# Kernel tuning notes

Measured on AMD Instinct MI355X. Metric: run time of the kernel, lower is better.

Reference implementation:

```python
import jax, jax.numpy as jnp
import numpy as np
from jax import lax

# Constants matching PostProcess(conf_thres=0.4, iou_thres=0.5, merge=False, agnostic=False)
CONF_THRES = 0.4
IOU_THRES = 0.5
MAX_WH = 4096.0   # per-class box offset (agnostic=False)
MAX_DET = 300     # hardcoded in module
MAX_NMS = 30000   # cap on NMS candidates (yolov5 convention); JAX needs static shapes
B, N, NC = 16, 25200, 80


def setup_inputs() -> dict:
    key = jax.random.key(0)
    u = jax.random.uniform(key, (B, N, 5 + NC), dtype=jnp.float32)
    # cx,cy in [0,640); w,h in [2,102); obj and class scores in [0,1)
    scale = jnp.concatenate([jnp.array([640.0, 640.0, 100.0, 100.0], jnp.float32),
                             jnp.ones((1 + NC,), jnp.float32)])
    shift = jnp.concatenate([jnp.array([0.0, 0.0, 2.0, 2.0], jnp.float32),
                             jnp.zeros((1 + NC,), jnp.float32)])
    prediction = u * scale + shift
    return {"prediction": prediction}


def _cxcywh_to_xyxy(x):
    cx, cy, w, h = x[..., 0], x[..., 1], x[..., 2], x[..., 3]
    return jnp.stack([cx - 0.5 * w, cy - 0.5 * h, cx + 0.5 * w, cy + 0.5 * h], axis=-1)


def _process_one(x):  # x: [N, 5+NC]
    obj = x[:, 4]
    cls_conf = x[:, 5:] * obj[:, None]          # x[:,5:] *= x[:,4:5]
    box = _cxcywh_to_xyxy(x[:, :4])             # [N, 4]
    # multi-label candidate mask: obj > conf AND class conf > conf (x[xc] then x[:,5:] > conf)
    cand = (obj[:, None] > CONF_THRES) & (cls_conf > CONF_THRES)   # [N, NC]
    flat = jnp.where(cand, cls_conf, 0.0).reshape(-1)              # [N*NC]
    top_scores, top_idx = lax.top_k(flat, MAX_NMS)                 # static-size candidate set
    bi = top_idx // NC                                             # box index i
    cj = (top_idx % NC).astype(jnp.float32)                        # class index j
    cand_boxes = box[bi]                                           # [M, 4]
    scores0 = jnp.where(top_scores > CONF_THRES, top_scores, 0.0)  # 0 marks invalid/suppressed
    off_boxes = cand_boxes + cj[:, None] * MAX_WH                  # per-class offset for NMS
    areas = (off_boxes[:, 2] - off_boxes[:, 0]) * (off_boxes[:, 3] - off_boxes[:, 1])
    idx_range = jnp.arange(MAX_NMS)

    def step(scores, _):
        # greedy NMS: pick best remaining, suppress IoU > thresh (torchvision semantics)
        idx = jnp.argmax(scores)
        s = scores[idx]
        keep = s > 0.0
        b = off_boxes[idx]
        lt = jnp.maximum(b[:2], off_boxes[:, :2])
        rb = jnp.minimum(b[2:], off_boxes[:, 2:])
        wh = jnp.clip(rb - lt, 0.0)
        inter = wh[:, 0] * wh[:, 1]
        iou = inter / (areas[idx] + areas - inter + 1e-9)
        suppress = (iou > IOU_THRES) | (idx_range == idx)
        return jnp.where(suppress, 0.0, scores), (idx, keep)

    _, (keep_idx, keep_flag) = lax.scan(step, scores0, None, length=MAX_DET)
    rows = jnp.concatenate([cand_boxes[keep_idx],
                            top_scores[keep_idx][:, None],
                            cj[keep_idx][:, None]], axis=1)        # [MAX_DET, 6] = xyxy, conf, cls
    return jnp.where(keep_flag[:, None], rows, 0.0)


def reference(prediction):
    # Padded fixed-shape analogue of torch.stack(output): [B, MAX_DET, 6], zero rows = no detection
    return jax.vmap(_process_one)(prediction)
```

## Files before the change

### kernel.cpp

```cpp
#include <hip/hip_runtime.h>
#include <stdint.h>

#define BATCH 16
#define NROW 25200
#define NCLS 80
#define ROWF 85
#define MAXDET 300
#define MAXNMS 30000u
#define NBIN 3072
#define BASEBITS 0x3EC00000u
#define CAP 32768u
#define BATCH_FLOATS 2142000

#define PREBIN 2048
#define NBUCK 1024
#define BUCKCAP 256

#define GATHER_MIN 512u
#define SORTCAP 1024
#define CH_SZ 128

#define TILE_ROWS 80
#define TILE_FLOATS 6800
#define RPB 400
#define SUBT 5
#define SBLK 63

#define ROWS_PER_BLK 256
#define SBLK2 99

__device__ __forceinline__ bool iou_gt_half(float ax1, float ay1, float ax2, float ay2, float aa,
                                            float bx1, float by1, float bx2, float by2, float ba) {
    float ltx = fmaxf(ax1, bx1), lty = fmaxf(ay1, by1);
    float rbx = fminf(ax2, bx2), rby = fminf(ay2, by2);
    float wx = fmaxf(__fsub_rn(rbx, ltx), 0.0f);
    float wy = fmaxf(__fsub_rn(rby, lty), 0.0f);
    float inter = __fmul_rn(wx, wy);
    float den = __fadd_rn(__fsub_rn(__fadd_rn(aa, ba), inter), 1e-9f);
    float t = __fmul_rn(0.5f, den);
    if (!(inter > t)) return false;
    float tg = __fmul_rn(0.50000012f, den);
    if (inter >= tg) return true;
    return __fdiv_rn(inter, den) > 0.5f;
}

__global__ __launch_bounds__(256) void k_stage(const float* __restrict__ pred,
                                               unsigned* __restrict__ bcnt,
                                               unsigned long long* __restrict__ bucket,
                                               unsigned* __restrict__ oflow,
                                               int staged) {
    if (!staged) return;
    int bx = blockIdx.x;
    int b = bx / SBLK2, blk = bx - b * SBLK2;
    int t = threadIdx.x, lane = t & 63, wv = t >> 6;
    const float* pb = pred + (size_t)b * BATCH_FLOATS;
    unsigned* bc = bcnt + (size_t)b * NBUCK;
    unsigned long long* bk = bucket + (size_t)b * NBUCK * BUCKCAP;
    int r0 = blk * ROWS_PER_BLK + wv * 64;
    int rown = NROW - r0;
    if (rown <= 0) return;
    if (rown > 64) rown = 64;
    float obj = 0.0f;
    if (lane < rown) obj = pb[(size_t)(r0 + lane) * ROWF + 4];
    unsigned long long live = __ballot(obj > 0.4f);
    while (live) {
        int j = (int)__builtin_ctzll(live);
        live &= live - 1ULL;
        float o = __shfl(obj, j);
        const float* rp = pb + (size_t)(r0 + j) * ROWF;
        unsigned grow = (unsigned)(r0 + j);
        {
            float cv = rp[5 + lane];
            float s = __fmul_rn(cv, o);
            if (s >= 0.75f) {
                unsigned bits = __float_as_uint(s);
                unsigned bin = (bits - BASEBITS) >> 12;
                if (bin > (unsigned)(NBIN - 1)) bin = NBIN - 1;
                unsigned bb = bin - PREBIN;
                unsigned pos = atomicAdd(&bc[bb], 1u);
                if (pos < (unsigned)BUCKCAP) {
                    unsigned flat = grow * (unsigned)NCLS + (unsigned)lane;
                    bk[(size_t)bb * BUCKCAP + pos] =
                        ((unsigned long long)bits << 32) |
                        (unsigned long long)(0xFFFFFFFFu - flat);
                } else oflow[b] = 1u;
            }
        }
        if (lane < 16) {
            int c = 64 + lane;
            float cv = rp[5 + c];
            float s = __fmul_rn(cv, o);
            if (s >= 0.75f) {
                unsigned bits = __float_as_uint(s);
                unsigned bin = (bits - BASEBITS) >> 12;
                if (bin > (unsigned)(NBIN - 1)) bin = NBIN - 1;
                unsigned bb = bin - PREBIN;
                unsigned pos = atomicAdd(&bc[bb], 1u);
                if (pos < (unsigned)BUCKCAP) {
                    unsigned flat = grow * (unsigned)NCLS + (unsigned)c;
                    bk[(size_t)bb * BUCKCAP + pos] =
                        ((unsigned long long)bits << 32) |
                        (unsigned long long)(0xFFFFFFFFu - flat);
                } else oflow[b] = 1u;
            }
        }
    }
}

__global__ __launch_bounds__(256) void k_prep(const unsigned* __restrict__ bcnt,
                                              const unsigned* __restrict__ oflow,
                                              unsigned* __restrict__ suf2,
                                              int* __restrict__ meta,
                                              int staged) {
    __shared__ unsigned sh[NBUCK];
    __shared__ unsigned sS[NBUCK];
    __shared__ unsigned cs[256];
    __shared__ int s_cut, s_need, s_tot;
    int b = blockIdx.x, t = threadIdx.x;
    const unsigned* bc = bcnt + (size_t)b * NBUCK;
    for (int i = t; i < NBUCK; i += 256) sh[i] = bc[i];
    if (t == 0) { s_cut = -1; s_need = 0; s_tot = 0; }
    __syncthreads();
    const int CHUNK = NBUCK / 256;
    int base = t * CHUNK;
    unsigned tot = 0;
    for (int i = 0; i < CHUNK; ++i) tot += sh[base + i];
    cs[t] = tot;
    __syncthreads();
    for (int off = 1; off < 256; off <<= 1) {
        unsigned v = (t + off < 256) ? cs[t + off] : 0u;
        __syncthreads();
        cs[t] += v;
        __syncthreads();
    }
    unsigned after = (t + 1 < 256) ? cs[t + 1] : 0u;
    for (int i = CHUNK - 1; i >= 0; --i) {
        after += sh[base + i];
        sS[base + i] = after;
    }
    __syncthreads();
    unsigned* g2 = suf2 + (size_t)b * (NBUCK + 1);
    for (int i = t; i < NBUCK; i += 256) g2[i] = sS[i];
    if (t == 0) g2[NBUCK] = 0u;
    for (int i = 0; i < CHUNK; ++i) {
        int v = base + i;
        unsigned Sv = sS[v];
        unsigned Sn = (v + 1 < NBUCK) ? sS[v + 1] : 0u;
        if (Sv >= MAXNMS && Sn < MAXNMS) {
            s_cut = PREBIN + v;
            s_need = (int)(MAXNMS - Sn);
            s_tot = (int)Sv;
        }
    }
    __syncthreads();
    if (t == 0) {
        int valid = (staged && s_cut >= 0 && sS[0] >= MAXNMS && oflow[b] == 0u) ? 1 : 0;
        meta[b * 4 + 0] = valid ? s_cut : 0;
        meta[b * 4 + 1] = valid ? s_need : 0;
        meta[b * 4 + 2] = valid ? s_tot : 0;
        meta[b * 4 + 3] = valid;
    }
}

__global__ __launch_bounds__(256) void k_hist_fb(const float* __restrict__ pred,
                                                 unsigned* __restrict__ hist,
                                                 const int* __restrict__ meta) {
    int bx = blockIdx.x;
    int b = bx / SBLK, blk = bx - b * SBLK;
    if (meta[b * 4 + 3]) return;
    __shared__ __align__(16) float rows[TILE_FLOATS];
    __shared__ unsigned shist[NBIN];
    int t = threadIdx.x, lane = t & 63, wv = t >> 6;
    for (int i = t; i < NBIN; i += 256) shist[i] = 0u;
    const float* pbase = pred + (size_t)b * BATCH_FLOATS + (size_t)blk * RPB * ROWF;
    for (int st = 0; st < SUBT; ++st) {
        __syncthreads();
        const float4* src = (const float4*)(pbase + (size_t)st * TILE_ROWS * ROWF);
        float4* dst = (float4*)rows;
        for (int i = t; i < TILE_FLOATS / 4; i += 256) dst[i] = src[i];
        __syncthreads();
        for (int r = wv; r < TILE_ROWS; r += 4) {
            float obj = rows[r * ROWF + 4];
            if (!(obj > 0.4f)) continue;
            for (int half = 0; half < 2; ++half) {
                int c = lane + (half << 6);
                if (c < NCLS) {
                    float cv = rows[r * ROWF + 5 + c];
                    float s = __fmul_rn(cv, obj);
                    if (s > 0.4f) {
                        unsigned bits = __float_as_uint(s);
                        unsigned bin = (bits - BASEBITS) >> 12;
                        if (bin > (unsigned)(NBIN - 1)) bin = NBIN - 1;
                        atomicAdd(&shist[bin], 1u);
                    }
                }
            }
        }
    }
    __syncthreads();
    unsigned* gh = hist + (size_t)b * NBIN;
    for (int i = t; i < NBIN; i += 256) {
        unsigned v = shist[i];
        if (v) atomicAdd(&gh[i], v);
    }
}

__global__ __launch_bounds__(256) void k_scan_fb(const unsigned* __restrict__ hist,
                                                 unsigned* __restrict__ suf,
                                                 int* __restrict__ meta) {
    int b = blockIdx.x, t = threadIdx.x;
    if (meta[b * 4 + 3]) return;
    __shared__ unsigned sh[NBIN];
    __shared__ unsigned sS[NBIN];
    __shared__ unsigned cs[256];
    __shared__ int s_cut, s_need, s_tot;
    const unsigned* gh = hist + (size_t)b * NBIN;
    for (int i = t; i < NBIN; i += 256) sh[i] = gh[i];
    if (t == 0) { s_cut = 0; s_need = 0x7FFFFFFF; s_tot = 0; }
    __syncthreads();
    const int CHUNK = NBIN / 256;
    int base = t * CHUNK;
    unsigned tot = 0;
    for (int i = 0; i < CHUNK; ++i) tot += sh[base + i];
    cs[t] = tot;
    __syncthreads();
    for (int off = 1; off < 256; off <<= 1) {
        unsigned v = (t + off < 256) ? cs[t + off] : 0u;
        __syncthreads();
        cs[t] += v;
        __syncthreads();
    }
    unsigned after = (t + 1 < 256) ? cs[t + 1] : 0u;
    for (int i = CHUNK - 1; i >= 0; --i) {
        after += sh[base + i];
        sS[base + i] = after;
    }
    __syncthreads();
    unsigned* gs = suf + (size_t)b * (NBIN + 1);
    for (int i = t; i < NBIN; i += 256) gs[i] = sS[i];
    if (t == 0) gs[NBIN] = 0u;
    for (int i = 0; i < CHUNK; ++i) {
        int v = base + i;
        unsigned Sv = sS[v];
        unsigned Sn = (v + 1 < NBIN) ? sS[v + 1] : 0u;
        if (Sv >= MAXNMS && Sn < MAXNMS) {
            s_cut = v;
            s_need = (int)(MAXNMS - Sn);
            s_tot = (int)Sv;
        }
    }
    __syncthreads();
    if (t == 0) {
        int cut = s_cut, needv = s_need, totv = s_tot;
        if (sS[0] < MAXNMS) { cut = 0; needv = 0x7FFFFFFF; totv = (int)sS[0]; }
        meta[b * 4 + 0] = cut;
        meta[b * 4 + 1] = needv;
        meta[b * 4 + 2] = totv;
    }
}

__global__ __launch_bounds__(256) void k_scatter_fb(const float* __restrict__ pred,
                                                    const unsigned* __restrict__ suf,
                                                    const int* __restrict__ meta,
                                                    unsigned* __restrict__ cursor,
                                                    unsigned long long* __restrict__ keys) {
    int bx = blockIdx.x;
    int b = bx / SBLK, blk = bx - b * SBLK;
    if (meta[b * 4 + 3]) return;
    __shared__ __align__(16) float rows[TILE_FLOATS];
    int t = threadIdx.x, lane = t & 63, wv = t >> 6;
    int cutbin = meta[b * 4 + 0];
    const float* pbase = pred + (size_t)b * BATCH_FLOATS + (size_t)blk * RPB * ROWF;
    unsigned rowbase0 = (unsigned)(blk * RPB);
    const unsigned* gs = suf + (size_t)b * (NBIN + 1);
    unsigned* cur = cursor + (size_t)b * NBIN;
    unsigned long long* kb = keys + (size_t)b * CAP;
    for (int st = 0; st < SUBT; ++st) {
        __syncthreads();
        const float4* src = (const float4*)(pbase + (size_t)st * TILE_ROWS * ROWF);
        float4* dst = (float4*)rows;
        for (int i = t; i < TILE_FLOATS / 4; i += 256) dst[i] = src[i];
        __syncthreads();
        for (int r = wv; r < TILE_ROWS; r += 4) {
            float obj = rows[r * ROWF + 4];
            if (!(obj > 0.4f)) continue;
            unsigned grow = rowbase0 + (unsigned)(st * TILE_ROWS + r);
            for (int half = 0; half < 2; ++half) {
                int c = lane + (half << 6);
                if (c < NCLS) {
                    float cv = rows[r * ROWF + 5 + c];
                    float s = __fmul_rn(cv, obj);
                    if (s > 0.4f) {
                        unsigned bits = __float_as_uint(s);
                        unsigned bin = (bits - BASEBITS) >> 12;
                        if (bin > (unsigned)(NBIN - 1)) bin = NBIN - 1;
                        if ((int)bin >= cutbin) {
                            unsigned pos = gs[bin + 1] + atomicAdd(&cur[bin], 1u);
                            if (pos < CAP) {
                                unsigned flat = grow * (unsigned)NCLS + (unsigned)c;
                                kb[pos] = ((unsigned long long)bits << 32) |
                                          (unsigned long long)(0xFFFFFFFFu - flat);
                            }
                        }
                    }
                }
            }
        }
    }
}

__global__ __launch_bounds__(1024) void k_nms(const float* __restrict__ pred,
                                              const unsigned* __restrict__ suf,
                                              const unsigned* __restrict__ suf2,
                                              const int* __restrict__ meta,
                                              const unsigned long long* __restrict__ keys,
                                              const unsigned long long* __restrict__ bucket,
                                              float* __restrict__ out) {
    __shared__ unsigned sgsL[NBUCK + 1];
    __shared__ unsigned long long ktmp[SORTCAP];
    __shared__ unsigned long long skeys[SORTCAP];
    __shared__ unsigned maskW[CH_SZ][5];
    __shared__ unsigned sup0w[4];
    __shared__ float cbox[CH_SZ][9];
    __shared__ float kept[MAXDET][5];
    __shared__ int klist[MAXDET];
    __shared__ int s_nk, s_localk;

    int b = blockIdx.x;
    int tid = threadIdx.x;
    int lane = tid & 63, wv = tid >> 6;

    int cutbin = meta[b * 4 + 0];
    int needv  = meta[b * 4 + 1];
    unsigned total = (unsigned)meta[b * 4 + 2];
    int valid  = meta[b * 4 + 3];
    if (total > CAP) total = CAP;
    const unsigned* gs = suf + (size_t)b * (NBIN + 1);
    const unsigned* g2 = suf2 + (size_t)b * (NBUCK + 1);
    const unsigned long long* kb = keys + (size_t)b * CAP;
    const unsigned long long* bk = bucket + (size_t)b * NBUCK * BUCKCAP;
    const float* pb = pred + (size_t)b * BATCH_FLOATS;
    float* ob = out + (size_t)b * MAXDET * 6;

    if (valid) for (int i = tid; i < NBUCK + 1; i += 1024) sgsL[i] = g2[i];
    if (tid == 0) s_nk = 0;
    __syncthreads();

    unsigned limit;
    if (needv == 0x7FFFFFFF) limit = total;
    else limit = (valid ? sgsL[cutbin + 1 - PREBIN] : gs[cutbin + 1]) + (unsigned)needv;
    if (limit > total) limit = total;

#define GSV(v) (valid ? sgsL[(v) - PREBIN] : gs[(v)])

    unsigned p = 0;
    while (p < limit) {
        if (s_nk >= MAXDET) break;

        int lo = cutbin, hi = NBIN - 1, w1 = cutbin;
        while (lo <= hi) { int mid = (lo + hi) >> 1;
            if (GSV(mid) > p) { w1 = mid; lo = mid + 1; } else hi = mid - 1; }
        lo = cutbin; hi = NBIN - 1; int w2 = cutbin;
        while (lo <= hi) { int mid = (lo + hi) >> 1;
            if (GSV(mid) >= p + GATHER_MIN) { w2 = mid; lo = mid + 1; } else hi = mid - 1; }
        unsigned gEnd = GSV(w2);
        if (gEnd <= p) gEnd = GSV(cutbin);
        if (gEnd - p > (unsigned)SORTCAP) {
            if (w2 < w1) gEnd = GSV(w2 + 1);
            if (gEnd - p > (unsigned)SORTCAP) gEnd = p + SORTCAP;
        }
        unsigned G = gEnd - p;

        unsigned myLo = 0, myHi = 0;
        unsigned long long raw = 0ULL;
        if (tid < (int)G) {
            unsigned idx = p + (unsigned)tid;
            int l2 = cutbin, h2 = NBIN - 1, v = cutbin;
            while (l2 <= h2) { int mid = (l2 + h2) >> 1;
                if (GSV(mid) > idx) { v = mid; l2 = mid + 1; } else h2 = mid - 1; }
            unsigned bstart = GSV(v + 1);
            unsigned bend = GSV(v);
            unsigned e = idx - bstart;
            raw = valid ? bk[(size_t)(v - PREBIN) * BUCKCAP + e] : kb[idx];
            myLo = bstart - p;
            myHi = bend - p; if (myHi > G) myHi = G;
            ktmp[tid] = raw;
        }
        __syncthreads();
        if (tid < (int)G) {
            unsigned rank = 0;
            for (unsigned u = myLo; u < myHi; ++u) rank += (ktmp[u] > raw) ? 1u : 0u;
            skeys[myLo + rank] = raw;
        }
        __syncthreads();

        unsigned consumable = limit - p; if (consumable > G) consumable = G;

        for (unsigned c0 = 0; c0 < consumable; c0 += CH_SZ) {
            int nk0 = s_nk;
            if (nk0 >= MAXDET) break;
            int CH = (int)((consumable - c0 < (unsigned)CH_SZ) ? (consumable - c0) : (unsigned)CH_SZ);

            if (tid < CH_SZ * 5) maskW[tid / 5][tid % 5] = 0u;
            if (tid >= CH_SZ * 5 && tid < CH_SZ * 5 + 4) sup0w[tid - CH_SZ * 5] = 0u;
            if (tid < CH) {
                unsigned long long kk = skeys[c0 + tid];
                unsigned flat = 0xFFFFFFFFu - (unsigned)kk;
                unsigned bi = flat / (unsigned)NCLS;
                unsigned cc = flat - bi * (unsigned)NCLS;
                const float* rp = pb + (size_t)bi * ROWF;
                float cx = rp[0], cy = rp[1], wd = rp[2], ht = rp[3];
                float hw = __fmul_rn(0.5f, wd), hh = __fmul_rn(0.5f, ht);
                float off = __fmul_rn((float)cc, 4096.0f);
                float x1 = __fsub_rn(cx, hw), y1 = __fsub_rn(cy, hh);
                float x2 = __fadd_rn(cx, hw), y2 = __fadd_rn(cy, hh);
                float ox1 = __fadd_rn(x1, off), oy1 = __fadd_rn(y1, off);
                float ox2 = __fadd_rn(x2, off), oy2 = __fadd_rn(y2, off);
                cbox[tid][0] = ox1; cbox[tid][1] = oy1;
                cbox[tid][2] = ox2; cbox[tid][3] = oy2;
                cbox[tid][4] = __fmul_rn(__fsub_rn(ox2, ox1), __fsub_rn(oy2, oy1));
            }
            __syncthreads();

            {
                int col = tid & (CH_SZ - 1);
                int part = tid >> 7;
                if (col < CH) {
                    float bx1 = cbox[col][0], by1 = cbox[col][1];
                    float bx2 = cbox[col][2], by2 = cbox[col][3], ba = cbox[col][4];
                    unsigned part16 = 0u;
                    int rbase = part << 4;
                    for (int k = 0; k < 16; ++k) {
                        int i2 = rbase + k;
                        if (i2 >= col || i2 >= CH) break;
                        if (iou_gt_half(cbox[i2][0], cbox[i2][1], cbox[i2][2], cbox[i2][3],
                                        cbox[i2][4], bx1, by1, bx2, by2, ba))
                            part16 |= (1u << k);
                    }
                    if (part16)
                        atomicOr(&maskW[col][part >> 1], part16 << ((part & 1) << 4));
                    bool f = false;
                    for (int k2 = part; k2 < nk0; k2 += 8) {
                        if (iou_gt_half(kept[k2][0], kept[k2][1], kept[k2][2], kept[k2][3],
                                        kept[k2][4], bx1, by1, bx2, by2, ba)) f = true;
                    }
                    if (f) atomicOr(&sup0w[col >> 5], 1u << (col & 31));
                }
            }
            __syncthreads();

            if (wv == 0) {
                unsigned keptw = 0u;
                int nkv = nk0, lk = 0;
                unsigned pre0 = (lane < 4 && CH > 0) ? maskW[0][lane] : 0u;
                unsigned pre1 = (lane < 4 && CH > 1) ? maskW[1][lane] : 0u;
                for (int j = 0; j < CH && nkv < MAXDET; ++j) {
                    unsigned colw = pre0;
                    pre0 = pre1;
                    pre1 = (lane < 4 && (j + 2) < CH) ? maskW[j + 2][lane] : 0u;
                    bool hit = (keptw & colw) != 0u;
                    bool sup = __any(hit);
                    if ((sup0w[j >> 5] >> (j & 31)) & 1u) sup = true;
                    if (!sup) {
                        if (lane == (j >> 5)) keptw |= 1u << (j & 31);
                        if (lane == 0) klist[lk] = j;
                        lk++; nkv++;
                    }
                }
                if (lane == 0) { s_localk = lk; s_nk = nkv; }
            }
            __syncthreads();

            int lk = s_localk;
            for (int t2 = tid; t2 < lk; t2 += 1024) {
                int i = klist[t2];
                int oidx = nk0 + t2;
                kept[oidx][0] = cbox[i][0]; kept[oidx][1] = cbox[i][1];
                kept[oidx][2] = cbox[i][2]; kept[oidx][3] = cbox[i][3];
                kept[oidx][4] = cbox[i][4];
                unsigned long long kk = skeys[c0 + i];
                unsigned bits = (unsigned)(kk >> 32);
                unsigned flat = 0xFFFFFFFFu - (unsigned)kk;
                unsigned bi = flat / (unsigned)NCLS;
                unsigned cc = flat - bi * (unsigned)NCLS;
                const float* rp = pb + (size_t)bi * ROWF;
                float cx = rp[0], cy = rp[1], wd = rp[2], ht = rp[3];
                float hw = __fmul_rn(0.5f, wd), hh = __fmul_rn(0.5f, ht);
                float* orow = ob + (size_t)oidx * 6;
                orow[0] = __fsub_rn(cx, hw);
                orow[1] = __fsub_rn(cy, hh);
                orow[2] = __fadd_rn(cx, hw);
                orow[3] = __fadd_rn(cy, hh);
                orow[4] = __uint_as_float(bits);
                orow[5] = (float)cc;
            }
            __syncthreads();
        }
        p = gEnd;
    }
#undef GSV
}

extern "C" void kernel_launch(void* const* d_in, const int* in_sizes, int n_in,
                              void* d_out, int out_size, void* d_ws, size_t ws_size,
                              hipStream_t stream) {
    const float* pred = (const float*)d_in[0];
    float* outp = (float*)d_out;
    char* ws = (char*)d_ws;

    const size_t OFF_KEYS = 0;
    const size_t SZ_KEYS  = (size_t)BATCH * CAP * 8;
    const size_t OFF_HIST = OFF_KEYS + SZ_KEYS;
    const size_t SZ_HIST  = (size_t)BATCH * NBIN * 4;
    const size_t OFF_CUR  = OFF_HIST + SZ_HIST;
    const size_t SZ_CUR   = (size_t)BATCH * NBIN * 4;
    const size_t OFF_BCNT = OFF_CUR + SZ_CUR;
    const size_t SZ_BCNT  = (size_t)BATCH * NBUCK * 4;
    const size_t OFF_OFLW = OFF_BCNT + SZ_BCNT;
    const size_t SZ_OFLW  = (size_t)BATCH * 4;
    const size_t OFF_META = OFF_OFLW + SZ_OFLW;
    const size_t SZ_META  = (size_t)BATCH * 4 * 4;
    const size_t OFF_SUF  = OFF_META + SZ_META;
    const size_t SZ_SUF   = (size_t)BATCH * (NBIN + 1) * 4;
    const size_t OFF_SUF2 = OFF_SUF + SZ_SUF;
    const size_t SZ_SUF2  = (size_t)BATCH * (NBUCK + 1) * 4;
    const size_t OFF_BUCK = OFF_SUF2 + SZ_SUF2;
    const size_t SZ_BUCK  = (size_t)BATCH * NBUCK * BUCKCAP * 8;
    const size_t WS_NEEDED = OFF_BUCK + SZ_BUCK;

    int staged = (ws_size >= WS_NEEDED) ? 1 : 0;

    unsigned long long* keys   = (unsigned long long*)(ws + OFF_KEYS);
    unsigned* hist             = (unsigned*)(ws + OFF_HIST);
    unsigned* cursor           = (unsigned*)(ws + OFF_CUR);
    unsigned* bcnt             = (unsigned*)(ws + OFF_BCNT);
    unsigned* oflow            = (unsigned*)(ws + OFF_OFLW);
    int* meta                  = (int*)(ws + OFF_META);
    unsigned* suf              = (unsigned*)(ws + OFF_SUF);
    unsigned* suf2             = (unsigned*)(ws + OFF_SUF2);
    unsigned long long* bucket = (unsigned long long*)(ws + OFF_BUCK);

    hipMemsetAsync(ws + OFF_HIST, 0, SZ_HIST + SZ_CUR + SZ_BCNT + SZ_OFLW + SZ_META, stream);
    hipMemsetAsync(d_out, 0, (size_t)out_size * sizeof(float), stream);

    k_stage<<<dim3(BATCH * SBLK2), dim3(256), 0, stream>>>(pred, bcnt, bucket, oflow, staged);
    k_prep<<<dim3(BATCH), dim3(256), 0, stream>>>(bcnt, oflow, suf2, meta, staged);
    k_hist_fb<<<dim3(BATCH * SBLK), dim3(256), 0, stream>>>(pred, hist, meta);
    k_scan_fb<<<dim3(BATCH), dim3(256), 0, stream>>>(hist, suf, meta);
    k_scatter_fb<<<dim3(BATCH * SBLK), dim3(256), 0, stream>>>(pred, suf, meta, cursor, keys);
    k_nms<<<dim3(BATCH), dim3(1024), 0, stream>>>(pred, suf, suf2, meta, keys, bucket, outp);
}
```

Measured before the change: 360.4 us.

## Replace global bucket atomics with per-block shared histograms and compact candidate list

The staging kernel now builds a per-block shared-memory histogram and a local key buffer, then writes per-block histograms and appends its keys to one compact per-batch candidate array with a single global atomic. k_prep sums the per-block histograms and checks that no bucket exceeds the sort capacity. In the staged path, the NMS kernel rescans the whole candidate list for each window, filters keys by bin range, and ranks them within their bin. This removes heavy global atomic contention and the large sparse bucket array. The cost is a full candidate scan per window inside the single-block-per-batch NMS kernel, plus extra histogram traffic.

```diff
diff --git a/kernel.cpp b/kernel.cpp
--- a/kernel.cpp
+++ b/kernel.cpp
@@ -14,7 +14,8 @@
 
 #define PREBIN 2048
 #define NBUCK 1024
-#define BUCKCAP 256
+#define CANDCAP 131072u
+#define KMAX 2048u
 
 #define GATHER_MIN 512u
 #define SORTCAP 1024
@@ -44,70 +45,93 @@
     return __fdiv_rn(inter, den) > 0.5f;
 }
 
+__device__ __forceinline__ unsigned bin_of_bits(unsigned bits) {
+    unsigned v = (bits - BASEBITS) >> 12;
+    if (v > (unsigned)(NBIN - 1)) v = NBIN - 1;
+    return v;
+}
+
 __global__ __launch_bounds__(256) void k_stage(const float* __restrict__ pred,
-                                               unsigned* __restrict__ bcnt,
-                                               unsigned long long* __restrict__ bucket,
+                                               unsigned* __restrict__ ghist,
+                                               unsigned* __restrict__ ccnt,
+                                               unsigned long long* __restrict__ cand,
                                                unsigned* __restrict__ oflow,
                                                int staged) {
     if (!staged) return;
+    __shared__ unsigned shist[NBUCK];
+    __shared__ unsigned long long skey[KMAX];
+    __shared__ unsigned s_cnt, s_n, s_base;
     int bx = blockIdx.x;
     int b = bx / SBLK2, blk = bx - b * SBLK2;
     int t = threadIdx.x, lane = t & 63, wv = t >> 6;
+    for (int i = t; i < NBUCK; i += 256) shist[i] = 0u;
+    if (t == 0) s_cnt = 0u;
+    __syncthreads();
     const float* pb = pred + (size_t)b * BATCH_FLOATS;
-    unsigned* bc = bcnt + (size_t)b * NBUCK;
-    unsigned long long* bk = bucket + (size_t)b * NBUCK * BUCKCAP;
     int r0 = blk * ROWS_PER_BLK + wv * 64;
     int rown = NROW - r0;
-    if (rown <= 0) return;
-    if (rown > 64) rown = 64;
-    float obj = 0.0f;
-    if (lane < rown) obj = pb[(size_t)(r0 + lane) * ROWF + 4];
-    unsigned long long live = __ballot(obj > 0.4f);
-    while (live) {
-        int j = (int)__builtin_ctzll(live);
-        live &= live - 1ULL;
-        float o = __shfl(obj, j);
-        const float* rp = pb + (size_t)(r0 + j) * ROWF;
-        unsigned grow = (unsigned)(r0 + j);
-        {
-            float cv = rp[5 + lane];
-            float s = __fmul_rn(cv, o);
-            if (s >= 0.75f) {
-                unsigned bits = __float_as_uint(s);
-                unsigned bin = (bits - BASEBITS) >> 12;
-                if (bin > (unsigned)(NBIN - 1)) bin = NBIN - 1;
-                unsigned bb = bin - PREBIN;
-                unsigned pos = atomicAdd(&bc[bb], 1u);
-                if (pos < (unsigned)BUCKCAP) {
+    if (rown > 0) {
+        if (rown > 64) rown = 64;
+        float obj = 0.0f;
+        if (lane < rown) obj = pb[(size_t)(r0 + lane) * ROWF + 4];
+        unsigned long long live = __ballot(obj > 0.4f);
+        while (live) {
+            int j = (int)__builtin_ctzll(live);
+            live &= live - 1ULL;
+            float o = __shfl(obj, j);
+            const float* rp = pb + (size_t)(r0 + j) * ROWF;
+            unsigned grow = (unsigned)(r0 + j);
+            {
+                float s = __fmul_rn(rp[5 + lane], o);
+                if (s >= 0.75f) {
+                    unsigned bits = __float_as_uint(s);
+                    unsigned bin = bin_of_bits(bits);
+                    atomicAdd(&shist[bin - PREBIN], 1u);
+                    unsigned u = atomicAdd(&s_cnt, 1u);
                     unsigned flat = grow * (unsigned)NCLS + (unsigned)lane;
-                    bk[(size_t)bb * BUCKCAP + pos] =
-                        ((unsigned long long)bits << 32) |
-                        (unsigned long long)(0xFFFFFFFFu - flat);
-                } else oflow[b] = 1u;
-            }
-        }
-        if (lane < 16) {
-            int c = 64 + lane;
-            float cv = rp[5 + c];
-            float s = __fmul_rn(cv, o);
-            if (s >= 0.75f) {
-                unsigned bits = __float_as_uint(s);
-                unsigned bin = (bits - BASEBITS) >> 12;
-                if (bin > (unsigned)(NBIN - 1)) bin = NBIN - 1;
-                unsigned bb = bin - PREBIN;
-                unsigned pos = atomicAdd(&bc[bb], 1u);
-                if (pos < (unsigned)BUCKCAP) {
+                    if (u < KMAX)
+                        skey[u] = ((unsigned long long)bits << 32) |
+                                  (unsigned long long)(0xFFFFFFFFu - flat);
+                    else oflow[b] = 1u;
+                }
+            }
+            if (lane < 16) {
+                int c = 64 + lane;
+                float s = __fmul_rn(rp[5 + c], o);
+                if (s >= 0.75f) {
+                    unsigned bits = __float_as_uint(s);
+                    unsigned bin = bin_of_bits(bits);
+                    atomicAdd(&shist[bin - PREBIN], 1u);
+                    unsigned u = atomicAdd(&s_cnt, 1u);
                     unsigned flat = grow * (unsigned)NCLS + (unsigned)c;
-                    bk[(size_t)bb * BUCKCAP + pos] =
-                        ((unsigned long long)bits << 32) |
-                        (unsigned long long)(0xFFFFFFFFu - flat);
-                } else oflow[b] = 1u;
-            }
-        }
-    }
-}
-
-__global__ __launch_bounds__(256) void k_prep(const unsigned* __restrict__ bcnt,
+                    if (u < KMAX)
+                        skey[u] = ((unsigned long long)bits << 32) |
+                                  (unsigned long long)(0xFFFFFFFFu - flat);
+                    else oflow[b] = 1u;
+                }
+            }
+        }
+    }
+    __syncthreads();
+    unsigned* gh = ghist + (size_t)(b * SBLK2 + blk) * NBUCK;
+    for (int i = t; i < NBUCK; i += 256) gh[i] = shist[i];
+    if (t == 0) {
+        unsigned n = s_cnt;
+        if (n > KMAX) n = KMAX;
+        unsigned base = atomicAdd(&ccnt[b], n);
+        if (base + n > CANDCAP) oflow[b] = 1u;
+        s_n = n; s_base = base;
+    }
+    __syncthreads();
+    unsigned n = s_n, base = s_base;
+    if (base + n <= CANDCAP) {
+        unsigned long long* cd = cand + (size_t)b * CANDCAP + base;
+        for (unsigned k = t; k < n; k += 256) cd[k] = skey[k];
+    }
+}
+
+__global__ __launch_bounds__(256) void k_prep(const unsigned* __restrict__ ghist,
+                                              const unsigned* __restrict__ ccnt,
                                               const unsigned* __restrict__ oflow,
                                               unsigned* __restrict__ suf2,
                                               int* __restrict__ meta,
@@ -116,11 +140,18 @@
     __shared__ unsigned sS[NBUCK];
     __shared__ unsigned cs[256];
     __shared__ int s_cut, s_need, s_tot;
+    __shared__ unsigned s_bad;
     int b = blockIdx.x, t = threadIdx.x;
-    const unsigned* bc = bcnt + (size_t)b * NBUCK;
-    for (int i = t; i < NBUCK; i += 256) sh[i] = bc[i];
-    if (t == 0) { s_cut = -1; s_need = 0; s_tot = 0; }
-    __syncthreads();
+    for (int i = t; i < NBUCK; i += 256) {
+        unsigned s = 0;
+        const unsigned* g = ghist + (size_t)b * SBLK2 * NBUCK + i;
+        for (int k = 0; k < SBLK2; ++k) s += g[(size_t)k * NBUCK];
+        sh[i] = s;
+    }
+    if (t == 0) { s_cut = -1; s_need = 0; s_tot = 0; s_bad = 0u; }
+    __syncthreads();
+    for (int i = t; i < NBUCK; i += 256)
+        if (sh[i] > (unsigned)SORTCAP) atomicOr(&s_bad, 1u);
     const int CHUNK = NBUCK / 256;
     int base = t * CHUNK;
     unsigned tot = 0;
@@ -154,7 +185,8 @@
     }
     __syncthreads();
     if (t == 0) {
-        int valid = (staged && s_cut >= 0 && sS[0] >= MAXNMS && oflow[b] == 0u) ? 1 : 0;
+        int valid = (staged && s_cut >= 0 && s_bad == 0u &&
+                     oflow[b] == 0u && ccnt[b] <= CANDCAP) ? 1 : 0;
         meta[b * 4 + 0] = valid ? s_cut : 0;
         meta[b * 4 + 1] = valid ? s_need : 0;
         meta[b * 4 + 2] = valid ? s_tot : 0;
@@ -187,12 +219,7 @@
                 if (c < NCLS) {
                     float cv = rows[r * ROWF + 5 + c];
                     float s = __fmul_rn(cv, obj);
-                    if (s > 0.4f) {
-                        unsigned bits = __float_as_uint(s);
-                        unsigned bin = (bits - BASEBITS) >> 12;
-                        if (bin > (unsigned)(NBIN - 1)) bin = NBIN - 1;
-                        atomicAdd(&shist[bin], 1u);
-                    }
+                    if (s > 0.4f) atomicAdd(&shist[bin_of_bits(__float_as_uint(s))], 1u);
                 }
             }
         }
@@ -292,8 +319,7 @@
                     float s = __fmul_rn(cv, obj);
                     if (s > 0.4f) {
                         unsigned bits = __float_as_uint(s);
-                        unsigned bin = (bits - BASEBITS) >> 12;
-                        if (bin > (unsigned)(NBIN - 1)) bin = NBIN - 1;
+                        unsigned bin = bin_of_bits(bits);
                         if ((int)bin >= cutbin) {
                             unsigned pos = gs[bin + 1] + atomicAdd(&cur[bin], 1u);
                             if (pos < CAP) {
@@ -313,8 +339,9 @@
                                               const unsigned* __restrict__ suf,
                                               const unsigned* __restrict__ suf2,
                                               const int* __restrict__ meta,
+                                              const unsigned* __restrict__ ccnt,
                                               const unsigned long long* __restrict__ keys,
-                                              const unsigned long long* __restrict__ bucket,
+                                              const unsigned long long* __restrict__ cand,
                                               float* __restrict__ out) {
     __shared__ unsigned sgsL[NBUCK + 1];
     __shared__ unsigned long long ktmp[SORTCAP];
@@ -325,6 +352,7 @@
     __shared__ float kept[MAXDET][5];
     __shared__ int klist[MAXDET];
     __shared__ int s_nk, s_localk;
+    __shared__ unsigned s_gc;
 
     int b = blockIdx.x;
     int tid = threadIdx.x;
@@ -334,11 +362,13 @@
     int needv  = meta[b * 4 + 1];
     unsigned total = (unsigned)meta[b * 4 + 2];
     int valid  = meta[b * 4 + 3];
-    if (total > CAP) total = CAP;
+    if (!valid && total > CAP) total = CAP;
     const unsigned* gs = suf + (size_t)b * (NBIN + 1);
     const unsigned* g2 = suf2 + (size_t)b * (NBUCK + 1);
     const unsigned long long* kb = keys + (size_t)b * CAP;
-    const unsigned long long* bk = bucket + (size_t)b * NBUCK * BUCKCAP;
+    const unsigned long long* cd = cand + (size_t)b * CANDCAP;
+    unsigned ccb = valid ? ccnt[b] : 0u;
+    if (ccb > CANDCAP) ccb = CANDCAP;
     const float* pb = pred + (size_t)b * BATCH_FLOATS;
     float* ob = out + (size_t)b * MAXDET * 6;
 
@@ -346,12 +376,12 @@
     if (tid == 0) s_nk = 0;
     __syncthreads();
 
+#define GSV(v) (valid ? sgsL[(v) - PREBIN] : gs[(v)])
+
     unsigned limit;
     if (needv == 0x7FFFFFFF) limit = total;
-    else limit = (valid ? sgsL[cutbin + 1 - PREBIN] : gs[cutbin + 1]) + (unsigned)needv;
+    else limit = GSV(cutbin + 1) + (unsigned)needv;
     if (limit > total) limit = total;
-
-#define GSV(v) (valid ? sgsL[(v) - PREBIN] : gs[(v)])
 
     unsigned p = 0;
     while (p < limit) {
@@ -371,28 +401,55 @@
         }
         unsigned G = gEnd - p;
 
-        unsigned myLo = 0, myHi = 0;
-        unsigned long long raw = 0ULL;
-        if (tid < (int)G) {
-            unsigned idx = p + (unsigned)tid;
-            int l2 = cutbin, h2 = NBIN - 1, v = cutbin;
-            while (l2 <= h2) { int mid = (l2 + h2) >> 1;
-                if (GSV(mid) > idx) { v = mid; l2 = mid + 1; } else h2 = mid - 1; }
-            unsigned bstart = GSV(v + 1);
-            unsigned bend = GSV(v);
-            unsigned e = idx - bstart;
-            raw = valid ? bk[(size_t)(v - PREBIN) * BUCKCAP + e] : kb[idx];
-            myLo = bstart - p;
-            myHi = bend - p; if (myHi > G) myHi = G;
-            ktmp[tid] = raw;
-        }
-        __syncthreads();
-        if (tid < (int)G) {
-            unsigned rank = 0;
-            for (unsigned u = myLo; u < myHi; ++u) rank += (ktmp[u] > raw) ? 1u : 0u;
-            skeys[myLo + rank] = raw;
-        }
-        __syncthreads();
+        if (valid) {
+            if (tid == 0) s_gc = 0u;
+            __syncthreads();
+            for (unsigned k = tid; k < ccb; k += 1024) {
+                unsigned long long key = cd[k];
+                unsigned v = bin_of_bits((unsigned)(key >> 32));
+                if ((int)v >= w2 && (int)v <= w1) {
+                    unsigned u = atomicAdd(&s_gc, 1u);
+                    if (u < (unsigned)SORTCAP) ktmp[u] = key;
+                }
+            }
+            __syncthreads();
+            unsigned Gc = s_gc; if (Gc > (unsigned)SORTCAP) Gc = (unsigned)SORTCAP;
+            if (tid < (int)Gc) {
+                unsigned long long key = ktmp[tid];
+                unsigned v = bin_of_bits((unsigned)(key >> 32));
+                unsigned bstart = GSV(v + 1);
+                unsigned rank = 0;
+                for (unsigned u = 0; u < Gc; ++u) {
+                    unsigned long long kk = ktmp[u];
+                    unsigned vu = bin_of_bits((unsigned)(kk >> 32));
+                    rank += (vu == v && kk > key) ? 1u : 0u;
+                }
+                skeys[(bstart - p) + rank] = key;
+            }
+            __syncthreads();
+        } else {
+            unsigned myLo = 0, myHi = 0;
+            unsigned long long raw = 0ULL;
+            if (tid < (int)G) {
+                unsigned idx = p + (unsigned)tid;
+                int l2 = cutbin, h2 = NBIN - 1, v = cutbin;
+                while (l2 <= h2) { int mid = (l2 + h2) >> 1;
+                    if (GSV(mid) > idx) { v = mid; l2 = mid + 1; } else h2 = mid - 1; }
+                unsigned bstart = GSV(v + 1);
+                unsigned bend = GSV(v);
+                raw = kb[idx];
+                myLo = bstart - p;
+                myHi = bend - p; if (myHi > G) myHi = G;
+                ktmp[tid] = raw;
+            }
+            __syncthreads();
+            if (tid < (int)G) {
+                unsigned rank = 0;
+                for (unsigned u = myLo; u < myHi; ++u) rank += (ktmp[u] > raw) ? 1u : 0u;
+                skeys[myLo + rank] = raw;
+            }
+            __syncthreads();
+        }
 
         unsigned consumable = limit - p; if (consumable > G) consumable = G;
 
@@ -508,45 +565,49 @@
     float* outp = (float*)d_out;
     char* ws = (char*)d_ws;
 
-    const size_t OFF_KEYS = 0;
-    const size_t SZ_KEYS  = (size_t)BATCH * CAP * 8;
-    const size_t OFF_HIST = OFF_KEYS + SZ_KEYS;
+    const size_t OFF_HIST = 0;
     const size_t SZ_HIST  = (size_t)BATCH * NBIN * 4;
     const size_t OFF_CUR  = OFF_HIST + SZ_HIST;
     const size_t SZ_CUR   = (size_t)BATCH * NBIN * 4;
-    const size_t OFF_BCNT = OFF_CUR + SZ_CUR;
-    const size_t SZ_BCNT  = (size_t)BATCH * NBUCK * 4;
-    const size_t OFF_OFLW = OFF_BCNT + SZ_BCNT;
+    const size_t OFF_CCNT = OFF_CUR + SZ_CUR;
+    const size_t SZ_CCNT  = (size_t)BATCH * 4;
+    const size_t OFF_OFLW = OFF_CCNT + SZ_CCNT;
     const size_t SZ_OFLW  = (size_t)BATCH * 4;
     const size_t OFF_META = OFF_OFLW + SZ_OFLW;
     const size_t SZ_META  = (size_t)BATCH * 4 * 4;
-    const size_t OFF_SUF  = OFF_META + SZ_META;
+    const size_t ZERO_SZ  = OFF_META + SZ_META;
+    const size_t OFF_SUF  = ZERO_SZ;
     const size_t SZ_SUF   = (size_t)BATCH * (NBIN + 1) * 4;
     const size_t OFF_SUF2 = OFF_SUF + SZ_SUF;
     const size_t SZ_SUF2  = (size_t)BATCH * (NBUCK + 1) * 4;
-    const size_t OFF_BUCK = OFF_SUF2 + SZ_SUF2;
-    const size_t SZ_BUCK  = (size_t)BATCH * NBUCK * BUCKCAP * 8;
-    const size_t WS_NEEDED = OFF_BUCK + SZ_BUCK;
+    const size_t OFF_KEYS = OFF_SUF2 + SZ_SUF2;
+    const size_t SZ_KEYS  = (size_t)BATCH * CAP * 8;
+    const size_t OFF_GH   = OFF_KEYS + SZ_KEYS;
+    const size_t SZ_GH    = (size_t)BATCH * SBLK2 * NBUCK * 4;
+    const size_t OFF_CAND = OFF_GH + SZ_GH;
+    const size_t SZ_CAND  = (size_t)BATCH * CANDCAP * 8;
+    const size_t WS_NEEDED = OFF_CAND + SZ_CAND;
 
     int staged = (ws_size >= WS_NEEDED) ? 1 : 0;
 
-    unsigned long long* keys   = (unsigned long long*)(ws + OFF_KEYS);
     unsigned* hist             = (unsigned*)(ws + OFF_HIST);
     unsigned* cursor           = (unsigned*)(ws + OFF_CUR);
-    unsigned* bcnt             = (unsigned*)(ws + OFF_BCNT);
+    unsigned* ccnt             = (unsigned*)(ws + OFF_CCNT);
     unsigned* oflow            = (unsigned*)(ws + OFF_OFLW);
     int* meta                  = (int*)(ws + OFF_META);
     unsigned* suf              = (unsigned*)(ws + OFF_SUF);
     unsigned* suf2             = (unsigned*)(ws + OFF_SUF2);
-    unsigned long long* bucket = (unsigned long long*)(ws + OFF_BUCK);
-
-    hipMemsetAsync(ws + OFF_HIST, 0, SZ_HIST + SZ_CUR + SZ_BCNT + SZ_OFLW + SZ_META, stream);
+    unsigned long long* keys   = (unsigned long long*)(ws + OFF_KEYS);
+    unsigned* ghist            = (unsigned*)(ws + OFF_GH);
+    unsigned long long* cand   = (unsigned long long*)(ws + OFF_CAND);
+
+    hipMemsetAsync(ws, 0, ZERO_SZ, stream);
     hipMemsetAsync(d_out, 0, (size_t)out_size * sizeof(float), stream);
 
-    k_stage<<<dim3(BATCH * SBLK2), dim3(256), 0, stream>>>(pred, bcnt, bucket, oflow, staged);
-    k_prep<<<dim3(BATCH), dim3(256), 0, stream>>>(bcnt, oflow, suf2, meta, staged);
+    k_stage<<<dim3(BATCH * SBLK2), dim3(256), 0, stream>>>(pred, ghist, ccnt, cand, oflow, staged);
+    k_prep<<<dim3(BATCH), dim3(256), 0, stream>>>(ghist, ccnt, oflow, suf2, meta, staged);
     k_hist_fb<<<dim3(BATCH * SBLK), dim3(256), 0, stream>>>(pred, hist, meta);
     k_scan_fb<<<dim3(BATCH), dim3(256), 0, stream>>>(hist, suf, meta);
     k_scatter_fb<<<dim3(BATCH * SBLK), dim3(256), 0, stream>>>(pred, suf, meta, cursor, keys);
-    k_nms<<<dim3(BATCH), dim3(1024), 0, stream>>>(pred, suf, suf2, meta, keys, bucket, outp);
-}
+    k_nms<<<dim3(BATCH), dim3(1024), 0, stream>>>(pred, suf, suf2, meta, ccnt, keys, cand, outp);
+}
```

New measurement: 375.2 us. 4.1% more time.
